# Performance work log

Measured on AMD Instinct MI355X. Metric: run time of the kernel, lower is better.

The kernel has to match this reference:

```python
import jax, jax.numpy as jnp
import numpy as np

H = 4          # hidden_size
NUM_LAYERS = 5
SEQ = 610
BATCH = 128


def _lstm_layer(x, w_i, w_h, bi, bh):
    # x: [B, T, I]; w_i: [4H, I]; w_h: [4H, H]; bi, bh: [4H]
    # PyTorch gate order: i, f, g, o
    B = x.shape[0]
    b = bi + bh

    def step(carry, xt):
        h, c = carry
        gates = xt @ w_i.T + h @ w_h.T + b          # [B, 4H]
        i, f, g, o = jnp.split(gates, 4, axis=-1)
        c = jax.nn.sigmoid(f) * c + jax.nn.sigmoid(i) * jnp.tanh(g)
        h = jax.nn.sigmoid(o) * jnp.tanh(c)
        return (h, c), h

    h0 = jnp.zeros((B, H), x.dtype)
    c0 = jnp.zeros((B, H), x.dtype)
    (_, _), hs = jax.lax.scan(step, (h0, c0), jnp.swapaxes(x, 0, 1))  # hs: [T, B, H]
    return jnp.swapaxes(hs, 0, 1)                   # [B, T, H]


def setup_inputs() -> dict:
    key = jax.random.key(0)
    ks = jax.random.split(key, 10)
    s = 1.0 / np.sqrt(H)  # PyTorch default uniform(-1/sqrt(H), 1/sqrt(H))
    u = lambda k, shape: jax.random.uniform(k, shape, jnp.float32, -s, s)
    return {
        "x": jax.random.normal(ks[0], (BATCH, SEQ, 2), jnp.float32),
        "w_ih0": u(ks[1], (4 * H, 2)),
        "w_ih": u(ks[2], (NUM_LAYERS - 1, 4 * H, H)),
        "w_hh": u(ks[3], (NUM_LAYERS, 4 * H, H)),
        "b_ih": u(ks[4], (NUM_LAYERS, 4 * H)),
        "b_hh": u(ks[5], (NUM_LAYERS, 4 * H)),
        "w_lin": u(ks[6], (1, H)),
        "b_lin": u(ks[7], (1,)),
        "w_fc": jax.random.uniform(ks[8], (5, SEQ), jnp.float32, -1.0 / np.sqrt(SEQ), 1.0 / np.sqrt(SEQ)),
        "b_fc": jax.random.uniform(ks[9], (5,), jnp.float32, -1.0 / np.sqrt(SEQ), 1.0 / np.sqrt(SEQ)),
    }


def reference(x, w_ih0, w_ih, w_hh, b_ih, b_hh, w_lin, b_lin, w_fc, b_fc):
    # 5-layer stacked LSTM, zero initial state (as on the module's first call)
    out = _lstm_layer(x, w_ih0, w_hh[0], b_ih[0], b_hh[0])
    for l in range(NUM_LAYERS - 1):
        out = _lstm_layer(out, w_ih[l], w_hh[l + 1], b_ih[l + 1], b_hh[l + 1])
    # per-timestep Linear(4 -> 1) then cat along dim 1 -> [B, T]
    t = (out @ w_lin.T + b_lin)[..., 0]             # [B, 610]
    return t @ w_fc.T + b_fc                         # [B, 5]
```

## Files before the change

### kernel.cpp

```cpp
#include <hip/hip_runtime.h>
#include <math.h>

#define H 4
#define NL 5
#define SEQ 610
#define BATCH 128
#define TICKS (SEQ + NL - 1)

template<int CTRL, bool BC>
__device__ __forceinline__ float dpp(float old_, float src) {
    return __int_as_float(__builtin_amdgcn_update_dpp(
        __float_as_int(old_), __float_as_int(src), CTRL, 0xF, 0xF, BC));
}

__global__ __launch_bounds__(64) void lstm_dpp_kernel(
    const float* __restrict__ x,
    const float* __restrict__ w_ih0,
    const float* __restrict__ w_ih,
    const float* __restrict__ w_hh,
    const float* __restrict__ b_ih,
    const float* __restrict__ b_hh,
    const float* __restrict__ w_lin,
    const float* __restrict__ b_lin,
    const float* __restrict__ w_fc,
    const float* __restrict__ b_fc,
    float* __restrict__ out)
{
    __shared__ float lds_x[2 * SEQ * 2];
    __shared__ float lds_wfc[5 * SEQ];

    const int lane = threadIdx.x;
    const int half = lane >> 5;
    const int r    = lane & 31;
    const int l    = r >> 2;
    const int k    = r & 3;
    const int lw   = l > 4 ? 4 : l;
    const bool is_l0 = (l == 0);
    const int  b   = blockIdx.x * 2 + half;

    #pragma unroll
    for (int hh = 0; hh < 2; ++hh) {
        const float4* src = (const float4*)(x + (size_t)(blockIdx.x * 2 + hh) * (SEQ * 2));
        float4* dst = (float4*)&lds_x[hh * (SEQ * 2)];
        for (int i = lane; i < (SEQ * 2) / 4; i += 64) dst[i] = src[i];
    }
    {
        const float2* src = (const float2*)w_fc;
        float2* dst = (float2*)lds_wfc;
        for (int i = lane; i < (5 * SEQ) / 2; i += 64) dst[i] = src[i];
    }
    __syncthreads();

    float wi[4][4], wh[4][4], bias[4];
    #pragma unroll
    for (int j = 0; j < 4; ++j) {
        const float s = (j == 2) ? 2.8853900817779268f
                                 : -1.4426950408889634f;
        const int row = j * H + k;
        if (lw == 0) {
            wi[j][0] = w_ih0[row * 2 + 0] * s;
            wi[j][1] = w_ih0[row * 2 + 1] * s;
            wi[j][2] = 0.f; wi[j][3] = 0.f;
        } else {
            const float4 v = *(const float4*)&w_ih[((lw - 1) * 16 + row) * 4];
            wi[j][0] = v.x * s; wi[j][1] = v.y * s; wi[j][2] = v.z * s; wi[j][3] = v.w * s;
        }
        const float4 u = *(const float4*)&w_hh[(lw * 16 + row) * 4];
        wh[j][0] = u.x * s; wh[j][1] = u.y * s; wh[j][2] = u.z * s; wh[j][3] = u.w * s;
        bias[j] = (b_ih[lw * 16 + row] + b_hh[lw * 16 + row]) * s;
    }
    const float wl0 = w_lin[0], wl1 = w_lin[1], wl2 = w_lin[2], wl3 = w_lin[3];
    const float bl  = b_lin[0];

    const int xbase = half * (SEQ * 2);
    const int wfcA_base = k * SEQ;

    float c = 0.f;
    float hq0 = 0.f, hq1 = 0.f, hq2 = 0.f, hq3 = 0.f;
    const float2 xv0 = *(const float2*)&lds_x[xbase];
    float xq0 = is_l0 ? xv0.x : 0.f;
    float xq1 = is_l0 ? xv0.y : 0.f;
    float xq2 = 0.f, xq3 = 0.f;
    float wfcA = 0.f, wfcB = 0.f;
    float accA = 0.f, accB = 0.f;

    #pragma unroll 2
    for (int tau = 0; tau < TICKS; ++tau) {
        int tn = tau + 1; tn = tn > SEQ - 1 ? SEQ - 1 : tn;
        const float2 nx = *(const float2*)&lds_x[xbase + tn * 2];
        int t4 = tau - 3; t4 = t4 < 0 ? 0 : (t4 > SEQ - 1 ? SEQ - 1 : t4);
        const float nwA = lds_wfc[wfcA_base + t4];
        const float nwB = lds_wfc[4 * SEQ + t4];

        float g[4];
        #pragma unroll
        for (int j = 0; j < 4; ++j) {
            float a = bias[j];
            a = fmaf(wi[j][0], xq0, a);
            a = fmaf(wi[j][1], xq1, a);
            a = fmaf(wi[j][2], xq2, a);
            a = fmaf(wi[j][3], xq3, a);
            a = fmaf(wh[j][0], hq0, a);
            a = fmaf(wh[j][1], hq1, a);
            a = fmaf(wh[j][2], hq2, a);
            a = fmaf(wh[j][3], hq3, a);
            g[j] = a;
        }
        const float Ai = 1.f + __builtin_amdgcn_exp2f(g[0]);
        const float Af = 1.f + __builtin_amdgcn_exp2f(g[1]);
        const float Dg = 1.f + __builtin_amdgcn_exp2f(g[2]);
        const float Ao = 1.f + __builtin_amdgcn_exp2f(g[3]);
        const float M   = Ai * Dg;
        const float den = M * Af;
        const float num = fmaf(c, M, Af * (Dg - 2.f));
        const float cn  = num * __builtin_amdgcn_rcpf(den);
        const unsigned tt = (unsigned)(tau - l);
        c = (tt < SEQ) ? cn : 0.f;
        const float Dc = 1.f + __builtin_amdgcn_exp2f(c * 2.8853900817779268f);
        const float h  = (Dc - 2.f) * __builtin_amdgcn_rcpf(Ao * Dc);

        const float q0 = dpp<0x00, true>(0.f, h);
        const float q1 = dpp<0x55, true>(0.f, h);
        const float q2 = dpp<0xAA, true>(0.f, h);
        const float q3 = dpp<0xFF, true>(0.f, h);

        float p0 = dpp<0x142, true>(0.f, q0); p0 = dpp<0x114, false>(p0, q0);
        float p1 = dpp<0x142, true>(0.f, q1); p1 = dpp<0x114, false>(p1, q1);
        float p2 = dpp<0x142, true>(0.f, q2); p2 = dpp<0x114, false>(p2, q2);
        float p3 = dpp<0x142, true>(0.f, q3); p3 = dpp<0x114, false>(p3, q3);

        float tval = fmaf(q3, wl3, bl);
        tval = fmaf(q2, wl2, tval);
        tval = fmaf(q1, wl1, tval);
        tval = fmaf(q0, wl0, tval);
        tval = (tt < SEQ) ? tval : 0.f;
        accA = fmaf(tval, wfcA, accA);
        accB = fmaf(tval, wfcB, accB);

        hq0 = q0; hq1 = q1; hq2 = q2; hq3 = q3;
        xq0 = is_l0 ? nx.x : p0;
        xq1 = is_l0 ? nx.y : p1;
        xq2 = is_l0 ? 0.f  : p2;
        xq3 = is_l0 ? 0.f  : p3;
        wfcA = nwA; wfcB = nwB;
    }

    if (r >= 16 && r < 20) {
        out[b * 5 + k] = accA + b_fc[k];
        if (k == 0) out[b * 5 + 4] = accB + b_fc[4];
    }
}

extern "C" void kernel_launch(void* const* d_in, const int* in_sizes, int n_in,
                              void* d_out, int out_size, void* d_ws, size_t ws_size,
                              hipStream_t stream)
{
    const float* x     = (const float*)d_in[0];
    const float* w_ih0 = (const float*)d_in[1];
    const float* w_ih  = (const float*)d_in[2];
    const float* w_hh  = (const float*)d_in[3];
    const float* b_ih  = (const float*)d_in[4];
    const float* b_hh  = (const float*)d_in[5];
    const float* w_lin = (const float*)d_in[6];
    const float* b_lin = (const float*)d_in[7];
    const float* w_fc  = (const float*)d_in[8];
    const float* b_fc  = (const float*)d_in[9];
    float* out = (float*)d_out;

    lstm_dpp_kernel<<<dim3(BATCH / 2), dim3(64), 0, stream>>>(
        x, w_ih0, w_ih, w_hh, b_ih, b_hh, w_lin, b_lin, w_fc, b_fc, out);
}
```

Baseline: 187.6 us.

## Process two batch rows per lane with packed float2 math and software-pipelined loads

Each lane now carries two independent batch rows in 2-wide vectors, so packed FMA instructions can be used and the two dependency chains interleave to hide latency. The grid is halved to 32 workgroups. The input-projection term is computed one step ahead, off the recurrent critical path. LDS loads are prefetched two ticks in advance, and the tt<SEQ gating is dropped in the steady-state loop. The cost is that half as many wavefronts run in parallel, and the per-tick chain on each wave gets longer if the packing does not pay off.

```diff
diff --git a/kernel.cpp b/kernel.cpp
--- a/kernel.cpp
+++ b/kernel.cpp
@@ -7,13 +7,36 @@
 #define BATCH 128
 #define TICKS (SEQ + NL - 1)
 
+typedef float v2f __attribute__((ext_vector_type(2)));
+
+#if __has_builtin(__builtin_elementwise_fma)
+#define FMA2(a, b, c) __builtin_elementwise_fma((a), (b), (c))
+#else
+static __device__ __forceinline__ v2f FMA2(v2f a, v2f b, v2f c) {
+    v2f r; r[0] = fmaf(a[0], b[0], c[0]); r[1] = fmaf(a[1], b[1], c[1]); return r;
+}
+#endif
+
 template<int CTRL, bool BC>
-__device__ __forceinline__ float dpp(float old_, float src) {
+__device__ __forceinline__ float dpp1(float old_, float src) {
     return __int_as_float(__builtin_amdgcn_update_dpp(
         __float_as_int(old_), __float_as_int(src), CTRL, 0xF, 0xF, BC));
 }
-
-__global__ __launch_bounds__(64) void lstm_dpp_kernel(
+template<int CTRL, bool BC>
+__device__ __forceinline__ v2f dpp2(v2f old_, v2f src) {
+    v2f r;
+    r[0] = dpp1<CTRL, BC>(old_[0], src[0]);
+    r[1] = dpp1<CTRL, BC>(old_[1], src[1]);
+    return r;
+}
+__device__ __forceinline__ v2f exp22(v2f a) {
+    v2f r; r[0] = __builtin_amdgcn_exp2f(a[0]); r[1] = __builtin_amdgcn_exp2f(a[1]); return r;
+}
+__device__ __forceinline__ v2f rcp2(v2f a) {
+    v2f r; r[0] = __builtin_amdgcn_rcpf(a[0]); r[1] = __builtin_amdgcn_rcpf(a[1]); return r;
+}
+
+__global__ __launch_bounds__(64) void lstm_2s_kernel(
     const float* __restrict__ x,
     const float* __restrict__ w_ih0,
     const float* __restrict__ w_ih,
@@ -26,8 +49,8 @@
     const float* __restrict__ b_fc,
     float* __restrict__ out)
 {
-    __shared__ float lds_x[2 * SEQ * 2];
-    __shared__ float lds_wfc[5 * SEQ];
+    __shared__ float lds_x[4 * SEQ * 2 + 24];
+    __shared__ float lds_wfc[5 * SEQ + 16];
 
     const int lane = threadIdx.x;
     const int half = lane >> 5;
@@ -36,12 +59,13 @@
     const int k    = r & 3;
     const int lw   = l > 4 ? 4 : l;
     const bool is_l0 = (l == 0);
-    const int  b   = blockIdx.x * 2 + half;
+    const int rowA = blockIdx.x * 4 + half;
+    const int rowB = rowA + 2;
 
     #pragma unroll
-    for (int hh = 0; hh < 2; ++hh) {
-        const float4* src = (const float4*)(x + (size_t)(blockIdx.x * 2 + hh) * (SEQ * 2));
-        float4* dst = (float4*)&lds_x[hh * (SEQ * 2)];
+    for (int rr = 0; rr < 4; ++rr) {
+        const float4* src = (const float4*)(x + (size_t)(blockIdx.x * 4 + rr) * (SEQ * 2));
+        float4* dst = (float4*)&lds_x[rr * (SEQ * 2)];
         for (int i = lane; i < (SEQ * 2) / 4; i += 64) dst[i] = src[i];
     }
     {
@@ -51,103 +75,138 @@
     }
     __syncthreads();
 
-    float wi[4][4], wh[4][4], bias[4];
+    v2f wi2[4][4], wh2[4][4], bias2[4];
     #pragma unroll
     for (int j = 0; j < 4; ++j) {
         const float s = (j == 2) ? 2.8853900817779268f
                                  : -1.4426950408889634f;
         const int row = j * H + k;
+        float a0, a1, a2, a3;
         if (lw == 0) {
-            wi[j][0] = w_ih0[row * 2 + 0] * s;
-            wi[j][1] = w_ih0[row * 2 + 1] * s;
-            wi[j][2] = 0.f; wi[j][3] = 0.f;
+            a0 = w_ih0[row * 2 + 0] * s; a1 = w_ih0[row * 2 + 1] * s; a2 = 0.f; a3 = 0.f;
         } else {
             const float4 v = *(const float4*)&w_ih[((lw - 1) * 16 + row) * 4];
-            wi[j][0] = v.x * s; wi[j][1] = v.y * s; wi[j][2] = v.z * s; wi[j][3] = v.w * s;
+            a0 = v.x * s; a1 = v.y * s; a2 = v.z * s; a3 = v.w * s;
         }
+        wi2[j][0] = (v2f){a0, a0}; wi2[j][1] = (v2f){a1, a1};
+        wi2[j][2] = (v2f){a2, a2}; wi2[j][3] = (v2f){a3, a3};
         const float4 u = *(const float4*)&w_hh[(lw * 16 + row) * 4];
-        wh[j][0] = u.x * s; wh[j][1] = u.y * s; wh[j][2] = u.z * s; wh[j][3] = u.w * s;
-        bias[j] = (b_ih[lw * 16 + row] + b_hh[lw * 16 + row]) * s;
-    }
-    const float wl0 = w_lin[0], wl1 = w_lin[1], wl2 = w_lin[2], wl3 = w_lin[3];
-    const float bl  = b_lin[0];
-
-    const int xbase = half * (SEQ * 2);
-    const int wfcA_base = k * SEQ;
-
-    float c = 0.f;
-    float hq0 = 0.f, hq1 = 0.f, hq2 = 0.f, hq3 = 0.f;
-    const float2 xv0 = *(const float2*)&lds_x[xbase];
-    float xq0 = is_l0 ? xv0.x : 0.f;
-    float xq1 = is_l0 ? xv0.y : 0.f;
-    float xq2 = 0.f, xq3 = 0.f;
-    float wfcA = 0.f, wfcB = 0.f;
-    float accA = 0.f, accB = 0.f;
-
-    #pragma unroll 2
-    for (int tau = 0; tau < TICKS; ++tau) {
-        int tn = tau + 1; tn = tn > SEQ - 1 ? SEQ - 1 : tn;
-        const float2 nx = *(const float2*)&lds_x[xbase + tn * 2];
-        int t4 = tau - 3; t4 = t4 < 0 ? 0 : (t4 > SEQ - 1 ? SEQ - 1 : t4);
-        const float nwA = lds_wfc[wfcA_base + t4];
-        const float nwB = lds_wfc[4 * SEQ + t4];
-
-        float g[4];
-        #pragma unroll
-        for (int j = 0; j < 4; ++j) {
-            float a = bias[j];
-            a = fmaf(wi[j][0], xq0, a);
-            a = fmaf(wi[j][1], xq1, a);
-            a = fmaf(wi[j][2], xq2, a);
-            a = fmaf(wi[j][3], xq3, a);
-            a = fmaf(wh[j][0], hq0, a);
-            a = fmaf(wh[j][1], hq1, a);
-            a = fmaf(wh[j][2], hq2, a);
-            a = fmaf(wh[j][3], hq3, a);
-            g[j] = a;
+        wh2[j][0] = (v2f){u.x * s, u.x * s}; wh2[j][1] = (v2f){u.y * s, u.y * s};
+        wh2[j][2] = (v2f){u.z * s, u.z * s}; wh2[j][3] = (v2f){u.w * s, u.w * s};
+        const float bb = (b_ih[lw * 16 + row] + b_hh[lw * 16 + row]) * s;
+        bias2[j] = (v2f){bb, bb};
+    }
+    v2f wl2[4], bl2;
+    #pragma unroll
+    for (int j = 0; j < 4; ++j) wl2[j] = (v2f){w_lin[j], w_lin[j]};
+    bl2 = (v2f){b_lin[0], b_lin[0]};
+
+    const int xbA = half * (SEQ * 2);
+    const int xbB = (2 + half) * (SEQ * 2);
+    const int wbase  = k * SEQ;
+    const int w4base = 4 * SEQ;
+    const v2f z2 = (v2f){0.f, 0.f};
+
+    v2f c2 = z2, q0 = z2, q1 = z2, q2 = z2, q3 = z2;
+    v2f accA2 = z2, accB2 = z2, wfcA2 = z2, wfcB2 = z2;
+    v2f pre0, pre1, pre2, pre3;
+    {
+        v2f xq0 = (v2f){is_l0 ? lds_x[xbA + 0] : 0.f, is_l0 ? lds_x[xbB + 0] : 0.f};
+        v2f xq1 = (v2f){is_l0 ? lds_x[xbA + 1] : 0.f, is_l0 ? lds_x[xbB + 1] : 0.f};
+        pre0 = FMA2(wi2[0][1], xq1, FMA2(wi2[0][0], xq0, bias2[0]));
+        pre1 = FMA2(wi2[1][1], xq1, FMA2(wi2[1][0], xq0, bias2[1]));
+        pre2 = FMA2(wi2[2][1], xq1, FMA2(wi2[2][0], xq0, bias2[2]));
+        pre3 = FMA2(wi2[3][1], xq1, FMA2(wi2[3][0], xq0, bias2[3]));
+    }
+
+    #define CORE(tau_, GATED, NXA0, NXA1, NXB0, NXB1, NWA, NWB)                       \
+    {                                                                                 \
+        v2f G0 = FMA2(wh2[0][3], q3, FMA2(wh2[0][2], q2, FMA2(wh2[0][1], q1, FMA2(wh2[0][0], q0, pre0)))); \
+        v2f G1 = FMA2(wh2[1][3], q3, FMA2(wh2[1][2], q2, FMA2(wh2[1][1], q1, FMA2(wh2[1][0], q0, pre1)))); \
+        v2f G2 = FMA2(wh2[2][3], q3, FMA2(wh2[2][2], q2, FMA2(wh2[2][1], q1, FMA2(wh2[2][0], q0, pre2)))); \
+        v2f G3 = FMA2(wh2[3][3], q3, FMA2(wh2[3][2], q2, FMA2(wh2[3][1], q1, FMA2(wh2[3][0], q0, pre3)))); \
+        v2f Ai = exp22(G0) + 1.f;                                                     \
+        v2f Af = exp22(G1) + 1.f;                                                     \
+        v2f Dg = exp22(G2) + 1.f;                                                     \
+        v2f Ao = exp22(G3) + 1.f;                                                     \
+        v2f M   = Ai * Dg;                                                            \
+        v2f den = M * Af;                                                             \
+        v2f num = FMA2(c2, M, Af * (Dg - 2.f));                                       \
+        v2f cn  = num * rcp2(den);                                                    \
+        unsigned tt = (unsigned)((tau_) - l);                                         \
+        c2 = (GATED) ? ((tt < SEQ) ? cn : z2) : cn;                                   \
+        v2f Dc = exp22(c2 * 2.8853900817779268f) + 1.f;                               \
+        v2f h2 = (Dc - 2.f) * rcp2(Ao * Dc);                                          \
+        v2f nq0 = dpp2<0x00, true>(z2, h2);                                           \
+        v2f nq1 = dpp2<0x55, true>(z2, h2);                                           \
+        v2f nq2 = dpp2<0xAA, true>(z2, h2);                                           \
+        v2f nq3 = dpp2<0xFF, true>(z2, h2);                                           \
+        v2f p0 = dpp2<0x142, true>(z2, nq0); p0 = dpp2<0x114, false>(p0, nq0);        \
+        v2f p1 = dpp2<0x142, true>(z2, nq1); p1 = dpp2<0x114, false>(p1, nq1);        \
+        v2f p2 = dpp2<0x142, true>(z2, nq2); p2 = dpp2<0x114, false>(p2, nq2);        \
+        v2f p3 = dpp2<0x142, true>(z2, nq3); p3 = dpp2<0x114, false>(p3, nq3);        \
+        v2f nx0 = (v2f){NXA0, NXB0};                                                  \
+        v2f nx1 = (v2f){NXA1, NXB1};                                                  \
+        v2f xq0 = is_l0 ? nx0 : p0;                                                   \
+        v2f xq1 = is_l0 ? nx1 : p1;                                                   \
+        pre0 = FMA2(wi2[0][3], p3, FMA2(wi2[0][2], p2, FMA2(wi2[0][1], xq1, FMA2(wi2[0][0], xq0, bias2[0])))); \
+        pre1 = FMA2(wi2[1][3], p3, FMA2(wi2[1][2], p2, FMA2(wi2[1][1], xq1, FMA2(wi2[1][0], xq0, bias2[1])))); \
+        pre2 = FMA2(wi2[2][3], p3, FMA2(wi2[2][2], p2, FMA2(wi2[2][1], xq1, FMA2(wi2[2][0], xq0, bias2[2])))); \
+        pre3 = FMA2(wi2[3][3], p3, FMA2(wi2[3][2], p2, FMA2(wi2[3][1], xq1, FMA2(wi2[3][0], xq0, bias2[3])))); \
+        v2f tval = FMA2(nq3, wl2[3], bl2);                                            \
+        tval = FMA2(nq2, wl2[2], tval);                                               \
+        tval = FMA2(nq1, wl2[1], tval);                                               \
+        tval = FMA2(nq0, wl2[0], tval);                                               \
+        if (GATED) tval = (tt < SEQ) ? tval : z2;                                     \
+        accA2 = FMA2(tval, wfcA2, accA2);                                             \
+        accB2 = FMA2(tval, wfcB2, accB2);                                             \
+        q0 = nq0; q1 = nq1; q2 = nq2; q3 = nq3;                                       \
+        wfcA2 = (v2f){NWA, NWA};                                                      \
+        wfcB2 = (v2f){NWB, NWB};                                                      \
+    }
+
+    for (int tau = 0; tau < 4; ++tau) {
+        const int tn = tau + 1;
+        int t4 = tau - 3; t4 = t4 < 0 ? 0 : t4;
+        const float nxA0_ = lds_x[xbA + tn * 2], nxA1_ = lds_x[xbA + tn * 2 + 1];
+        const float nxB0_ = lds_x[xbB + tn * 2], nxB1_ = lds_x[xbB + tn * 2 + 1];
+        const float nwA_ = lds_wfc[wbase + t4], nwB_ = lds_wfc[w4base + t4];
+        CORE(tau, true, nxA0_, nxA1_, nxB0_, nxB1_, nwA_, nwB_);
+    }
+
+    float s0_nxA0 = lds_x[xbA + 5 * 2], s0_nxA1 = lds_x[xbA + 5 * 2 + 1];
+    float s0_nxB0 = lds_x[xbB + 5 * 2], s0_nxB1 = lds_x[xbB + 5 * 2 + 1];
+    float s0_wA = lds_wfc[wbase + 1], s0_wB = lds_wfc[w4base + 1];
+    float s1_nxA0 = lds_x[xbA + 6 * 2], s1_nxA1 = lds_x[xbA + 6 * 2 + 1];
+    float s1_nxB0 = lds_x[xbB + 6 * 2], s1_nxB1 = lds_x[xbB + 6 * 2 + 1];
+    float s1_wA = lds_wfc[wbase + 2], s1_wB = lds_wfc[w4base + 2];
+
+    #define TICK(tau_, SNXA0, SNXA1, SNXB0, SNXB1, SWA, SWB)                          \
+    {                                                                                 \
+        const int tpf = (tau_) + 3;                                                   \
+        const float t_nxA0 = lds_x[xbA + tpf * 2], t_nxA1 = lds_x[xbA + tpf * 2 + 1]; \
+        const float t_nxB0 = lds_x[xbB + tpf * 2], t_nxB1 = lds_x[xbB + tpf * 2 + 1]; \
+        const float t_wA = lds_wfc[wbase + (tau_) - 1];                               \
+        const float t_wB = lds_wfc[w4base + (tau_) - 1];                              \
+        CORE(tau_, false, SNXA0, SNXA1, SNXB0, SNXB1, SWA, SWB);                      \
+        SNXA0 = t_nxA0; SNXA1 = t_nxA1; SNXB0 = t_nxB0; SNXB1 = t_nxB1;               \
+        SWA = t_wA; SWB = t_wB;                                                       \
+    }
+
+    for (int tau = 4; tau < TICKS; tau += 2) {
+        TICK(tau,     s0_nxA0, s0_nxA1, s0_nxB0, s0_nxB1, s0_wA, s0_wB);
+        TICK(tau + 1, s1_nxA0, s1_nxA1, s1_nxB0, s1_nxB1, s1_wA, s1_wB);
+    }
+    #undef TICK
+    #undef CORE
+
+    if (r >= 16 && r < 20) {
+        out[rowA * 5 + k] = accA2[0] + b_fc[k];
+        out[rowB * 5 + k] = accA2[1] + b_fc[k];
+        if (k == 0) {
+            out[rowA * 5 + 4] = accB2[0] + b_fc[4];
+            out[rowB * 5 + 4] = accB2[1] + b_fc[4];
         }
-        const float Ai = 1.f + __builtin_amdgcn_exp2f(g[0]);
-        const float Af = 1.f + __builtin_amdgcn_exp2f(g[1]);
-        const float Dg = 1.f + __builtin_amdgcn_exp2f(g[2]);
-        const float Ao = 1.f + __builtin_amdgcn_exp2f(g[3]);
-        const float M   = Ai * Dg;
-        const float den = M * Af;
-        const float num = fmaf(c, M, Af * (Dg - 2.f));
-        const float cn  = num * __builtin_amdgcn_rcpf(den);
-        const unsigned tt = (unsigned)(tau - l);
-        c = (tt < SEQ) ? cn : 0.f;
-        const float Dc = 1.f + __builtin_amdgcn_exp2f(c * 2.8853900817779268f);
-        const float h  = (Dc - 2.f) * __builtin_amdgcn_rcpf(Ao * Dc);
-
-        const float q0 = dpp<0x00, true>(0.f, h);
-        const float q1 = dpp<0x55, true>(0.f, h);
-        const float q2 = dpp<0xAA, true>(0.f, h);
-        const float q3 = dpp<0xFF, true>(0.f, h);
-
-        float p0 = dpp<0x142, true>(0.f, q0); p0 = dpp<0x114, false>(p0, q0);
-        float p1 = dpp<0x142, true>(0.f, q1); p1 = dpp<0x114, false>(p1, q1);
-        float p2 = dpp<0x142, true>(0.f, q2); p2 = dpp<0x114, false>(p2, q2);
-        float p3 = dpp<0x142, true>(0.f, q3); p3 = dpp<0x114, false>(p3, q3);
-
-        float tval = fmaf(q3, wl3, bl);
-        tval = fmaf(q2, wl2, tval);
-        tval = fmaf(q1, wl1, tval);
-        tval = fmaf(q0, wl0, tval);
-        tval = (tt < SEQ) ? tval : 0.f;
-        accA = fmaf(tval, wfcA, accA);
-        accB = fmaf(tval, wfcB, accB);
-
-        hq0 = q0; hq1 = q1; hq2 = q2; hq3 = q3;
-        xq0 = is_l0 ? nx.x : p0;
-        xq1 = is_l0 ? nx.y : p1;
-        xq2 = is_l0 ? 0.f  : p2;
-        xq3 = is_l0 ? 0.f  : p3;
-        wfcA = nwA; wfcB = nwB;
-    }
-
-    if (r >= 16 && r < 20) {
-        out[b * 5 + k] = accA + b_fc[k];
-        if (k == 0) out[b * 5 + 4] = accB + b_fc[4];
     }
 }
 
@@ -167,6 +226,6 @@
     const float* b_fc  = (const float*)d_in[9];
     float* out = (float*)d_out;
 
-    lstm_dpp_kernel<<<dim3(BATCH / 2), dim3(64), 0, stream>>>(
+    lstm_2s_kernel<<<dim3(BATCH / 4), dim3(64), 0, stream>>>(
         x, w_ih0, w_ih, w_hh, b_ih, b_hh, w_lin, b_lin, w_fc, b_fc, out);
 }
```

After: 222.8 us. 1.19x slower.
